# Kernel tuning notes

Hardware: AMD Instinct MI355X
Metric: run time of the kernel (lower is better)

Reference implementation:

```python
import jax, jax.numpy as jnp
import numpy as np
from jax import lax

B, C, H, W = 64, 1, 256, 256
N = H * W
K = 16384  # positive_trials
LOG_CLAMP = -100.0  # torch BCELoss clamps log terms at -100


def setup_inputs() -> dict:
    key = jax.random.key(0)
    k1, k2, k3 = jax.random.split(key, 3)
    decision_scores = jax.random.normal(k1, (B, N, 2), dtype=jnp.float32)
    s_map = jax.random.uniform(k2, (B, C, H, W), dtype=jnp.float32)
    # gumbel noise g = -log(-log(U)), matching F.gumbel_softmax sampling
    u = jax.random.uniform(k3, (B, N, 2), dtype=jnp.float32, minval=1e-10, maxval=1.0)
    gumbel_noise = -jnp.log(-jnp.log(u))
    return {"decision_scores": decision_scores, "s_map": s_map, "gumbel_noise": gumbel_noise}


def reference(decision_scores, s_map, gumbel_noise):
    # Tokenizer: b c h w -> b (h w) c
    tokens = jnp.transpose(s_map.reshape(B, C, H * W), (0, 2, 1))  # [B, N, 1]
    # soft gumbel-softmax (tau=1, hard=False), keep prob of class 0
    soft = jax.nn.softmax(decision_scores + gumbel_noise, axis=-1)[:, :, 0:1]  # [B, N, 1]
    # top-K salient token indices per sample (descending sort -> top_k)
    _, idx = lax.top_k(tokens[:, :, 0], K)  # [B, K]
    trials = jnp.zeros((B, N), dtype=tokens.dtype)
    trials = trials.at[jnp.arange(B)[:, None], idx].set(1.0)[:, :, None]  # [B, N, 1]
    # BCE with reduction='sum', log clamped at -100 like torch
    log_p = jnp.clip(jnp.log(soft), LOG_CLAMP, None)
    log_1mp = jnp.clip(jnp.log(1.0 - soft), LOG_CLAMP, None)
    loss = -jnp.sum(trials * log_p + (1.0 - trials) * log_1mp)
    return loss
```

## Files before the change

kernel.cpp:

```cpp
#include <hip/hip_runtime.h>
#include <cstdint>

#define BATCH 64
#define NPIX 65536
#define TOPK 16384
#define NB 256
#define SEGS 32
#define WLO 186
#define WHI 198
#define NWBIN (WHI - WLO + 1)
#define CAPB 192
#define NSLOT (SEGS * CAPB)
#define FCAP 1024
#define WHSTRIDE 16

__device__ __forceinline__ float block_reduce(float acc) {
    __shared__ float w[4];
    __syncthreads();
    #pragma unroll
    for (int off = 32; off > 0; off >>= 1) acc += __shfl_down(acc, off, 64);
    if ((threadIdx.x & 63) == 0) w[threadIdx.x >> 6] = acc;
    __syncthreads();
    return w[0] + w[1] + w[2] + w[3];
}

__device__ __forceinline__ float block_reduce1k(float acc) {
    __shared__ float w[16];
    __syncthreads();
    #pragma unroll
    for (int off = 32; off > 0; off >>= 1) acc += __shfl_down(acc, off, 64);
    if ((threadIdx.x & 63) == 0) w[threadIdx.x >> 6] = acc;
    __syncthreads();
    float s = 0.f;
    #pragma unroll
    for (int i = 0; i < 16; ++i) s += w[i];
    return s;
}

__device__ __forceinline__ void bce_from_d(float d, float& lp, float& llp) {
    float t = __logf(1.f + __expf(-fabsf(d)));
    lp  = fmaxf(fminf(d, 0.f) - t, -100.f);
    llp = fmaxf(-fmaxf(d, 0.f) - t, -100.f);
}

__device__ __forceinline__ int vkey(float v) {
    return (int)fminf(v * 256.0f, 255.0f);
}

__device__ __forceinline__ void stage_candidate(
    bool inwin, float v, uint32_t pix, float diff, int lane,
    uint32_t* ccount, uint32_t* bvb, uint32_t* bvi, uint32_t* bvd)
{
    unsigned long long m = __ballot(inwin);
    if (m == 0ull) return;
    uint32_t cnt = (uint32_t)__popcll(m);
    int leader = (int)__builtin_ctzll(m);
    uint32_t base = 0u;
    if (lane == leader) base = atomicAdd(ccount, cnt);
    base = (uint32_t)__shfl((int)base, leader, 64);
    if (inwin) {
        uint32_t p = base + (uint32_t)__popcll(m & ((1ull << lane) - 1ull));
        if (p < CAPB) {
            bvb[p] = __float_as_uint(v);
            bvi[p] = pix;
            bvd[p] = __float_as_uint(diff);
        }
    }
}

__global__ __launch_bounds__(256, 8) void k1_pass(
    const float4* __restrict__ sc, const float4* __restrict__ gn,
    const float2* __restrict__ tokp,
    float* __restrict__ pk1, float* __restrict__ psel, float* __restrict__ phi,
    uint32_t* __restrict__ gcc,
    uint32_t* __restrict__ cvb, uint32_t* __restrict__ cvi,
    uint32_t* __restrict__ cvd, uint32_t* __restrict__ whist,
    float* __restrict__ wdsumg,
    float* __restrict__ out)
{
    __shared__ uint32_t bvb[CAPB], bvi[CAPB], bvd[CAPB];
    __shared__ uint32_t qvb[CAPB], qvi[CAPB], qvd[CAPB];
    __shared__ uint32_t sh_wh[NWBIN], sh_pref[NWBIN], sh_cur[NWBIN];
    __shared__ float    sh_wds[NWBIN];
    __shared__ uint32_t ccount;
    const int tid  = threadIdx.x;
    const int lane = tid & 63;
    if (tid < CAPB) { qvb[tid] = 0u; qvi[tid] = 0u; qvd[tid] = 0u; }
    if (tid < NWBIN) { sh_wh[tid] = 0u; sh_cur[tid] = 0u; sh_wds[tid] = 0.f; }
    if (tid == 0) { ccount = 0u; if (blockIdx.x == 0) out[0] = 0.f; }
    __syncthreads();

    const int b   = blockIdx.x >> 5;
    const int seg = blockIdx.x & (SEGS - 1);
    const int pairbase = b * (NPIX / 2) + seg * 1024;

    float4 S[4], G[4];
    float2 T[4];
    #pragma unroll
    for (int it = 0; it < 4; ++it) {
        int j = pairbase + it * 256 + tid;
        S[it] = sc[j];
        G[it] = gn[j];
        T[it] = tokp[j];
    }

    float acc = 0.f, asel = 0.f, chi = 0.f;
    #pragma unroll
    for (int it = 0; it < 4; ++it) {
        int px0 = (seg * 1024 + it * 256 + tid) * 2;
        {
            float d = (S[it].x + G[it].x) - (S[it].y + G[it].y);
            float lp, llp; bce_from_d(d, lp, llp);
            acc += llp;
            float diff = lp - llp;
            int k = vkey(T[it].x);
            bool hi = (k > WHI);
            asel += hi ? diff : 0.f;
            chi  += hi ? 1.f : 0.f;
            stage_candidate(!hi && (k >= WLO), T[it].x, (uint32_t)px0, diff,
                            lane, &ccount, bvb, bvi, bvd);
        }
        {
            float d = (S[it].z + G[it].z) - (S[it].w + G[it].w);
            float lp, llp; bce_from_d(d, lp, llp);
            acc += llp;
            float diff = lp - llp;
            int k = vkey(T[it].y);
            bool hi = (k > WHI);
            asel += hi ? diff : 0.f;
            chi  += hi ? 1.f : 0.f;
            stage_candidate(!hi && (k >= WLO), T[it].y, (uint32_t)(px0 + 1), diff,
                            lane, &ccount, bvb, bvi, bvd);
        }
    }
    __syncthreads();
    const uint32_t cc  = ccount;
    const uint32_t nsl = cc < CAPB ? cc : CAPB;
    if (tid < nsl) {
        int k = vkey(__uint_as_float(bvb[tid]));
        atomicAdd(&sh_wh[k - WLO], 1u);
    }
    __syncthreads();
    if (tid == 0) {
        uint32_t run = 0;
        #pragma unroll
        for (int i = 0; i < NWBIN; ++i) { sh_pref[i] = run; run += sh_wh[i]; }
    }
    __syncthreads();
    if (tid < nsl) {
        uint32_t vb = bvb[tid];
        int bin = vkey(__uint_as_float(vb)) - WLO;
        uint32_t pos = sh_pref[bin] + atomicAdd(&sh_cur[bin], 1u);
        qvb[pos] = vb;
        qvi[pos] = bvi[tid];
        qvd[pos] = bvd[tid];
        atomicAdd(&sh_wds[bin], __uint_as_float(bvd[tid]));
    }
    __syncthreads();
    const size_t cbase = (size_t)blockIdx.x * CAPB;
    if (tid < CAPB) {
        cvb[cbase + tid] = qvb[tid];
        cvi[cbase + tid] = qvi[tid];
        cvd[cbase + tid] = qvd[tid];
    }
    if (tid == 0) gcc[blockIdx.x] = cc;

    float t1 = block_reduce(acc);
    float t2 = block_reduce(asel);
    float t3 = block_reduce(chi);
    if (tid == 0) {
        pk1[blockIdx.x]  = t1;
        psel[blockIdx.x] = t2;
        phi[blockIdx.x]  = t3;
    }
    if (tid < NWBIN) {
        whist[(size_t)blockIdx.x * WHSTRIDE + tid]  = sh_wh[tid];
        wdsumg[(size_t)blockIdx.x * WHSTRIDE + tid] = sh_wds[tid];
    }
}

__global__ __launch_bounds__(1024) void k4_finalize(
    const uint32_t* __restrict__ cvb, const uint32_t* __restrict__ cvi,
    const uint32_t* __restrict__ cvd, const uint32_t* __restrict__ gcc,
    const float* __restrict__ pk1, const float* __restrict__ psel,
    const float* __restrict__ phi, const uint32_t* __restrict__ whist,
    const float* __restrict__ wdsumg,
    const float4* __restrict__ tok4,
    const float2* __restrict__ sc2, const float2* __restrict__ gn2,
    float* __restrict__ out)
{
    __shared__ uint32_t fvb[FCAP], fvi[FCAP];
    __shared__ float    fdf[FCAP];
    __shared__ uint32_t fh[NB];
    __shared__ uint32_t wc[NWBIN];
    __shared__ uint32_t segstart[SEGS], segcnt[SEGS];
    __shared__ uint32_t fcnt;
    __shared__ int      sh_sb, sh_ovf;
    __shared__ uint32_t sh_rem;

    const int b = blockIdx.x, tid = threadIdx.x;
    if (tid == 0) { fcnt = 0u; sh_sb = -1; sh_ovf = 0; sh_rem = 1u; }
    __syncthreads();

    if (tid < SEGS && gcc[b * SEGS + tid] > CAPB) sh_ovf = 1;
    if (tid < NWBIN) {
        uint32_t u = 0;
        #pragma unroll
        for (int s = 0; s < SEGS; ++s)
            u += whist[(size_t)(b * SEGS + s) * WHSTRIDE + tid];
        wc[tid] = u;
    }
    float chl = (tid < SEGS) ? phi[b * SEGS + tid] : 0.f;
    float chf = block_reduce1k(chl);
    if (tid == 0) {
        uint32_t cnt_hi = (uint32_t)(chf + 0.5f);
        if (cnt_hi >= TOPK) sh_ovf = 1;
        else {
            uint32_t cum = cnt_hi;
            int found = -1; uint32_t rem = 1u;
            for (int jj = WHI; jj >= WLO; --jj) {
                uint32_t nc = cum + wc[jj - WLO];
                if (nc >= TOPK) { found = jj; rem = TOPK - cum; break; }
                cum = nc;
            }
            if (found < 0) sh_ovf = 1;
            else { sh_sb = found; sh_rem = rem; }
        }
    }
    __syncthreads();

    bool fast = (sh_ovf == 0);
    const int sb  = sh_sb;
    const int sbi = sb - WLO;
    float fac = (tid < SEGS) ? pk1[b * SEGS + tid] : 0.f;

    if (fast) {
        if (tid < SEGS) fac += psel[b * SEGS + tid];
        if (tid < SEGS * WHSTRIDE) {
            int s = tid >> 4, bin = tid & 15;
            if (bin < NWBIN && bin > sbi)
                fac += wdsumg[(size_t)(b * SEGS + s) * WHSTRIDE + bin];
        }
        if (tid < SEGS) {
            uint32_t st = 0;
            for (int i = 0; i < sbi; ++i)
                st += whist[(size_t)(b * SEGS + tid) * WHSTRIDE + i];
            segstart[tid] = st;
            segcnt[tid]   = whist[(size_t)(b * SEGS + tid) * WHSTRIDE + sbi];
        }
        __syncthreads();
        {
            int g = tid >> 5, l32 = tid & 31;
            uint32_t c = segcnt[g];
            size_t sbase = (size_t)(b * SEGS + g) * CAPB + segstart[g];
            for (uint32_t i = l32; i < c; i += 32) {
                uint32_t p = atomicAdd(&fcnt, 1u);
                if (p < FCAP) {
                    fvb[p] = cvb[sbase + i];
                    fvi[p] = cvi[sbase + i] & (NPIX - 1);
                    fdf[p] = __uint_as_float(cvd[sbase + i]);
                }
            }
        }
        __syncthreads();
        if (fcnt > FCAP) fast = false;
        if (fast) {
            const uint32_t cnt = fcnt, rem = sh_rem;
            for (uint32_t j = tid; j < cnt; j += 1024) {
                const uint32_t mb = fvb[j], mi = fvi[j];
                uint32_t rank = 0;
                for (uint32_t i = 0; i < cnt; ++i) {
                    uint32_t ob = fvb[i];
                    rank += (ob > mb) || (ob == mb && fvi[i] < mi);
                }
                if (rank < rem) fac += fdf[j];
            }
        }
    }

    if (!fast) {
        fac = (tid < SEGS) ? pk1[b * SEGS + tid] : 0.f;
        for (int i = tid; i < NB; i += 1024) fh[i] = 0u;
        if (tid == 0) fcnt = 0u;
        __syncthreads();
        const float4* tbase = tok4 + (size_t)b * (NPIX / 4);
        for (int it = 0; it < NPIX / 4 / 1024; ++it) {
            float4 v = tbase[it * 1024 + tid];
            atomicAdd(&fh[vkey(v.x)], 1u);
            atomicAdd(&fh[vkey(v.y)], 1u);
            atomicAdd(&fh[vkey(v.z)], 1u);
            atomicAdd(&fh[vkey(v.w)], 1u);
        }
        __syncthreads();
        if (tid == 0) {
            uint32_t cum = 0; int bin = NB - 1;
            for (; bin > 0; --bin) {
                if (cum + fh[bin] >= TOPK) break;
                cum += fh[bin];
            }
            sh_sb = bin; sh_rem = TOPK - cum;
        }
        __syncthreads();
        const int sb2 = sh_sb; const uint32_t rem2 = sh_rem;
        for (int it = 0; it < NPIX / 4 / 1024; ++it) {
            int j = it * 1024 + tid;
            float4 v = tbase[j];
            int px = j * 4;
            float fv[4] = {v.x, v.y, v.z, v.w};
            #pragma unroll
            for (int q = 0; q < 4; ++q) {
                int k = vkey(fv[q]);
                if (k > sb2) {
                    size_t idx = (size_t)b * NPIX + (px + q);
                    float2 Sv = sc2[idx]; float2 Gv = gn2[idx];
                    float d = (Sv.x + Gv.x) - (Sv.y + Gv.y);
                    float lp, llp; bce_from_d(d, lp, llp);
                    fac += lp - llp;
                } else if (k == sb2) {
                    uint32_t p = atomicAdd(&fcnt, 1u);
                    if (p < FCAP) { fvb[p] = __float_as_uint(fv[q]); fvi[p] = (uint32_t)(px + q); }
                }
            }
        }
        __syncthreads();
        const uint32_t cnt2 = min(fcnt, (uint32_t)FCAP);
        for (uint32_t j = tid; j < cnt2; j += 1024) {
            const uint32_t mb = fvb[j], mi = fvi[j];
            uint32_t rank = 0;
            for (uint32_t i = 0; i < cnt2; ++i) {
                uint32_t ob = fvb[i];
                rank += (ob > mb) || (ob == mb && fvi[i] < mi);
            }
            if (rank < rem2) {
                size_t idx = (size_t)b * NPIX + (mi & (NPIX - 1));
                float2 Sv = sc2[idx]; float2 Gv = gn2[idx];
                float d = (Sv.x + Gv.x) - (Sv.y + Gv.y);
                float lp, llp; bce_from_d(d, lp, llp);
                fac += lp - llp;
            }
        }
    }

    float tot = block_reduce1k(fac);
    if (tid == 0) atomicAdd(out, -tot);
}

extern "C" void kernel_launch(void* const* d_in, const int* in_sizes, int n_in,
                              void* d_out, int out_size, void* d_ws, size_t ws_size,
                              hipStream_t stream) {
    const float* scores = (const float*)d_in[0];
    const float* smap   = (const float*)d_in[1];
    const float* gumbel = (const float*)d_in[2];
    float* out = (float*)d_out;

    char* ws = (char*)d_ws;
    float*    pk1   = (float*)ws;    ws += (size_t)BATCH * SEGS * 4;
    float*    psel  = (float*)ws;    ws += (size_t)BATCH * SEGS * 4;
    float*    phi   = (float*)ws;    ws += (size_t)BATCH * SEGS * 4;
    uint32_t* gcc   = (uint32_t*)ws; ws += (size_t)BATCH * SEGS * 4;
    uint32_t* cvb   = (uint32_t*)ws; ws += (size_t)BATCH * NSLOT * 4;
    uint32_t* cvi   = (uint32_t*)ws; ws += (size_t)BATCH * NSLOT * 4;
    uint32_t* cvd   = (uint32_t*)ws; ws += (size_t)BATCH * NSLOT * 4;
    uint32_t* whist = (uint32_t*)ws; ws += (size_t)BATCH * SEGS * WHSTRIDE * 4;
    float*    wdsum = (float*)ws;    ws += (size_t)BATCH * SEGS * WHSTRIDE * 4;

    k1_pass<<<BATCH * SEGS, 256, 0, stream>>>(
        (const float4*)scores, (const float4*)gumbel, (const float2*)smap,
        pk1, psel, phi, gcc, cvb, cvi, cvd, whist, wdsum, out);

    k4_finalize<<<BATCH, 1024, 0, stream>>>(
        cvb, cvi, cvd, gcc, pk1, psel, phi, whist, wdsum,
        (const float4*)smap, (const float2*)scores, (const float2*)gumbel, out);
}
```

Measured before the change: 117.3 us.

## Halve segments per batch, doubling per-block work, and fuse block reductions

Each block of the first kernel now processes 2048 pixel pairs, up from 1024, so each batch splits into 16 segments instead of 32. Candidate capacity per block grows to 320, with strided loops over it, and the finalize kernel regroups by 64 lanes per segment. The three separate block reductions are merged into one pass with a single pair of barriers. The launch-bounds occupancy hint drops to 4, which allows more registers for the larger unrolled load arrays. The aim is to cut per-block fixed overhead (init, histogram, scatter, partial writes) and the finalize work, at the cost of fewer blocks (1024) and less latency hiding.

```diff
diff --git a/kernel.cpp b/kernel.cpp
--- a/kernel.cpp
+++ b/kernel.cpp
@@ -5,23 +5,33 @@
 #define NPIX 65536
 #define TOPK 16384
 #define NB 256
-#define SEGS 32
+#define SEGS 16
 #define WLO 186
 #define WHI 198
 #define NWBIN (WHI - WLO + 1)
-#define CAPB 192
+#define CAPB 320
 #define NSLOT (SEGS * CAPB)
 #define FCAP 1024
 #define WHSTRIDE 16
-
-__device__ __forceinline__ float block_reduce(float acc) {
-    __shared__ float w[4];
-    __syncthreads();
-    #pragma unroll
-    for (int off = 32; off > 0; off >>= 1) acc += __shfl_down(acc, off, 64);
-    if ((threadIdx.x & 63) == 0) w[threadIdx.x >> 6] = acc;
-    __syncthreads();
-    return w[0] + w[1] + w[2] + w[3];
+#define ITERS 8
+
+__device__ __forceinline__ void block_reduce3(
+    float a, float b, float c, float* o0, float* o1, float* o2)
+{
+    __shared__ float w[12];
+    __syncthreads();
+    #pragma unroll
+    for (int off = 32; off > 0; off >>= 1) {
+        a += __shfl_down(a, off, 64);
+        b += __shfl_down(b, off, 64);
+        c += __shfl_down(c, off, 64);
+    }
+    int wid = threadIdx.x >> 6;
+    if ((threadIdx.x & 63) == 0) { w[wid] = a; w[wid + 4] = b; w[wid + 8] = c; }
+    __syncthreads();
+    *o0 = w[0] + w[1] + w[2] + w[3];
+    *o1 = w[4] + w[5] + w[6] + w[7];
+    *o2 = w[8] + w[9] + w[10] + w[11];
 }
 
 __device__ __forceinline__ float block_reduce1k(float acc) {
@@ -68,7 +78,7 @@
     }
 }
 
-__global__ __launch_bounds__(256, 8) void k1_pass(
+__global__ __launch_bounds__(256, 4) void k1_pass(
     const float4* __restrict__ sc, const float4* __restrict__ gn,
     const float2* __restrict__ tokp,
     float* __restrict__ pk1, float* __restrict__ psel, float* __restrict__ phi,
@@ -85,19 +95,19 @@
     __shared__ uint32_t ccount;
     const int tid  = threadIdx.x;
     const int lane = tid & 63;
-    if (tid < CAPB) { qvb[tid] = 0u; qvi[tid] = 0u; qvd[tid] = 0u; }
+    for (int i = tid; i < CAPB; i += 256) { qvb[i] = 0u; qvi[i] = 0u; qvd[i] = 0u; }
     if (tid < NWBIN) { sh_wh[tid] = 0u; sh_cur[tid] = 0u; sh_wds[tid] = 0.f; }
     if (tid == 0) { ccount = 0u; if (blockIdx.x == 0) out[0] = 0.f; }
     __syncthreads();
 
-    const int b   = blockIdx.x >> 5;
+    const int b   = blockIdx.x >> 4;
     const int seg = blockIdx.x & (SEGS - 1);
-    const int pairbase = b * (NPIX / 2) + seg * 1024;
-
-    float4 S[4], G[4];
-    float2 T[4];
-    #pragma unroll
-    for (int it = 0; it < 4; ++it) {
+    const int pairbase = b * (NPIX / 2) + seg * (ITERS * 256);
+
+    float4 S[ITERS], G[ITERS];
+    float2 T[ITERS];
+    #pragma unroll
+    for (int it = 0; it < ITERS; ++it) {
         int j = pairbase + it * 256 + tid;
         S[it] = sc[j];
         G[it] = gn[j];
@@ -106,8 +116,8 @@
 
     float acc = 0.f, asel = 0.f, chi = 0.f;
     #pragma unroll
-    for (int it = 0; it < 4; ++it) {
-        int px0 = (seg * 1024 + it * 256 + tid) * 2;
+    for (int it = 0; it < ITERS; ++it) {
+        int px0 = (seg * (ITERS * 256) + it * 256 + tid) * 2;
         {
             float d = (S[it].x + G[it].x) - (S[it].y + G[it].y);
             float lp, llp; bce_from_d(d, lp, llp);
@@ -136,8 +146,8 @@
     __syncthreads();
     const uint32_t cc  = ccount;
     const uint32_t nsl = cc < CAPB ? cc : CAPB;
-    if (tid < nsl) {
-        int k = vkey(__uint_as_float(bvb[tid]));
+    for (uint32_t i = tid; i < nsl; i += 256) {
+        int k = vkey(__uint_as_float(bvb[i]));
         atomicAdd(&sh_wh[k - WLO], 1u);
     }
     __syncthreads();
@@ -147,27 +157,26 @@
         for (int i = 0; i < NWBIN; ++i) { sh_pref[i] = run; run += sh_wh[i]; }
     }
     __syncthreads();
-    if (tid < nsl) {
-        uint32_t vb = bvb[tid];
+    for (uint32_t i = tid; i < nsl; i += 256) {
+        uint32_t vb = bvb[i];
         int bin = vkey(__uint_as_float(vb)) - WLO;
         uint32_t pos = sh_pref[bin] + atomicAdd(&sh_cur[bin], 1u);
         qvb[pos] = vb;
-        qvi[pos] = bvi[tid];
-        qvd[pos] = bvd[tid];
-        atomicAdd(&sh_wds[bin], __uint_as_float(bvd[tid]));
+        qvi[pos] = bvi[i];
+        qvd[pos] = bvd[i];
+        atomicAdd(&sh_wds[bin], __uint_as_float(bvd[i]));
     }
     __syncthreads();
     const size_t cbase = (size_t)blockIdx.x * CAPB;
-    if (tid < CAPB) {
-        cvb[cbase + tid] = qvb[tid];
-        cvi[cbase + tid] = qvi[tid];
-        cvd[cbase + tid] = qvd[tid];
+    for (int i = tid; i < CAPB; i += 256) {
+        cvb[cbase + i] = qvb[i];
+        cvi[cbase + i] = qvi[i];
+        cvd[cbase + i] = qvd[i];
     }
     if (tid == 0) gcc[blockIdx.x] = cc;
 
-    float t1 = block_reduce(acc);
-    float t2 = block_reduce(asel);
-    float t3 = block_reduce(chi);
+    float t1, t2, t3;
+    block_reduce3(acc, asel, chi, &t1, &t2, &t3);
     if (tid == 0) {
         pk1[blockIdx.x]  = t1;
         psel[blockIdx.x] = t2;
@@ -250,10 +259,10 @@
         }
         __syncthreads();
         {
-            int g = tid >> 5, l32 = tid & 31;
+            int g = tid >> 6, l64 = tid & 63;
             uint32_t c = segcnt[g];
             size_t sbase = (size_t)(b * SEGS + g) * CAPB + segstart[g];
-            for (uint32_t i = l32; i < c; i += 32) {
+            for (uint32_t i = l64; i < c; i += 64) {
                 uint32_t p = atomicAdd(&fcnt, 1u);
                 if (p < FCAP) {
                     fvb[p] = cvb[sbase + i];
```

New measurement: 119.3 us. About the same (+1.7%).
